# Performance work log

Hardware: AMD Instinct MI355X
Metric: run time of the kernel (lower is better)

## Reference

```python
import jax, jax.numpy as jnp
import numpy as np

N = 128       # SSM state size
L = 32768     # l_max / sequence length
DT_MIN, DT_MAX = 0.001, 0.1


def setup_inputs() -> dict:
    key = jax.random.key(0)
    ku, ka, kb, kc, ks = jax.random.split(key, 5)
    u = jax.random.normal(ku, (L,), dtype=jnp.float32)
    # lecun_normal: std = 1/sqrt(fan_in); shift A by -2I for stability over L powers
    A = jax.random.normal(ka, (N, N), dtype=jnp.float32) * (1.0 / np.sqrt(N)) - 2.0 * jnp.eye(N, dtype=jnp.float32)
    B = jax.random.normal(kb, (N, 1), dtype=jnp.float32)            # fan_in=1 -> std 1
    C = jax.random.normal(kc, (1, N), dtype=jnp.float32) * (1.0 / np.sqrt(N))
    D = jnp.ones((1,), dtype=jnp.float32)
    log_step = jax.random.uniform(ks, (1,), dtype=jnp.float32) * (np.log(DT_MAX) - np.log(DT_MIN)) + np.log(DT_MIN)
    return {"u": u, "A": A, "B": B, "C": C, "D": D, "log_step": log_step}


def discretize(a, b, step):
    # bilinear (Tustin) discretization, identical to the flax module
    i = jnp.eye(a.shape[0], dtype=a.dtype)
    bl = jnp.linalg.inv(i - (step / 2.0) * a)
    ab = bl @ (i + (step / 2.0) * a)
    bb = (bl * step) @ b
    return ab, bb


def k_conv(ab, bb, cb, l):
    # K[t] = cb @ ab^t @ bb  -- same math as the matrix_power list-comp,
    # computed with a single scan carrying x_t = ab^t @ bb  (N,1)
    def step(x, _):
        k_t = (cb @ x).reshape(())
        return ab @ x, k_t
    _, k = jax.lax.scan(step, bb, None, length=l)
    return k  # (l,)


def causal_convolution(u, k):
    l = u.shape[0]
    ud = jnp.fft.rfft(jnp.pad(u, (0, k.shape[0])))
    kd = jnp.fft.rfft(jnp.pad(k, (0, l)))
    return jnp.fft.irfft(ud * kd)[:l]


def reference(u, A, B, C, D, log_step):
    step = jnp.exp(log_step)
    ab, bb = discretize(A, B, step)
    K = k_conv(ab, bb, C, u.shape[0])
    return causal_convolution(u, K) + D * u
```

## Files before the change

kernel.cpp:

```cpp
#include <hip/hip_runtime.h>
#include <math.h>

#define L_SEQ 32768
#define PL 16384
#define GP 16384

typedef unsigned short u16;
typedef float f32x4 __attribute__((ext_vector_type(4)));
typedef short bf16x8 __attribute__((ext_vector_type(8)));
typedef u16 u16x4 __attribute__((ext_vector_type(4)));

__device__ __forceinline__ u16 f2bf(float x) {
  unsigned u = __float_as_uint(x);
  u = u + 0x7FFFu + ((u >> 16) & 1u);
  return (u16)(u >> 16);
}
__device__ __forceinline__ float bf2f(u16 h) {
  return __uint_as_float(((unsigned)h) << 16);
}
__device__ __forceinline__ int MIDX(int r, int c) {
  return (r << 7) + (c ^ ((r & 7) << 3));
}
__device__ __forceinline__ f32x4 MF(bf16x8 a, bf16x8 b, f32x4 c) {
  return __builtin_amdgcn_mfma_f32_16x16x32_bf16(a, b, c, 0, 0, 0);
}

template<int ASRC,int BSRC,int OUTM,int OUTG,int MODE>
__device__ void mm(u16* lds, const u16* gA, int aPl, const u16* gB, int bPl,
                   u16* gO, int oPl, int gOrow0, u16* gO2,
                   int Mrows, int N, float c3, const u16* gE, const u16* gEt) {
  u16* Mh = lds;          u16* Ml = lds + PL;
  u16* Th = lds + 2 * PL; u16* Tl = lds + 3 * PL;
  const int t = threadIdx.x, lane = t & 63;
  const int la = lane & 15, g = lane >> 4;
  const int w = t >> 6;
  const int r0 = (w >> 2) << 5, c0 = (w & 3) << 5;
  constexpr bool doA = (OUTM == 2) || (OUTG == 2) || (OUTG == 3);
  constexpr bool doT = (OUTM == 2) || (OUTG == 1) || (OUTG == 3);
  const bool act = (r0 < Mrows) && (c0 < N);

  __syncthreads();

  f32x4 acc[2][2], accT[2][2];
#pragma unroll
  for (int i = 0; i < 2; ++i)
#pragma unroll
    for (int j = 0; j < 2; ++j) {
      acc[i][j] = (f32x4){0.f, 0.f, 0.f, 0.f};
      accT[i][j] = (f32x4){0.f, 0.f, 0.f, 0.f};
    }

  if (act) {
    bf16x8 Ah[2][2], Al[2][2], Bh[2][2], Bl[2][2];
    auto load_stage = [&](int kb, int s) {
      const int kp = (kb << 5) + (g << 3);
#pragma unroll
      for (int fr = 0; fr < 2; ++fr) {
        const int ar = r0 + (fr << 4) + la;
        if constexpr (ASRC == 0) {
          Ah[s][fr] = *(const bf16x8*)(Mh + MIDX(ar, kp));
          Al[s][fr] = *(const bf16x8*)(Ml + MIDX(ar, kp));
        } else {
          Ah[s][fr] = *(const bf16x8*)(gA + ar * 128 + kp);
          Al[s][fr] = *(const bf16x8*)(gA + aPl + ar * 128 + kp);
        }
      }
#pragma unroll
      for (int fc = 0; fc < 2; ++fc) {
        const int bc = c0 + (fc << 4) + la;
        if constexpr (BSRC == 0) {
          Bh[s][fc] = *(const bf16x8*)(Th + MIDX(bc, kp));
          Bl[s][fc] = *(const bf16x8*)(Tl + MIDX(bc, kp));
        } else {
          Bh[s][fc] = *(const bf16x8*)(gB + bc * 128 + kp);
          Bl[s][fc] = *(const bf16x8*)(gB + bPl + bc * 128 + kp);
        }
      }
    };
    load_stage(0, 0);
#pragma unroll
    for (int kb = 0; kb < 4; ++kb) {
      const int cur = kb & 1;
      if (kb < 3) load_stage(kb + 1, cur ^ 1);
#pragma unroll
      for (int fr = 0; fr < 2; ++fr)
#pragma unroll
        for (int fc = 0; fc < 2; ++fc) {
          if constexpr (doA) {
            acc[fr][fc] = MF(Ah[cur][fr], Bh[cur][fc], acc[fr][fc]);
            acc[fr][fc] = MF(Ah[cur][fr], Bl[cur][fc], acc[fr][fc]);
            acc[fr][fc] = MF(Al[cur][fr], Bh[cur][fc], acc[fr][fc]);
          }
          if constexpr (doT) {
            accT[fr][fc] = MF(Bh[cur][fc], Ah[cur][fr], accT[fr][fc]);
            accT[fr][fc] = MF(Bh[cur][fc], Al[cur][fr], accT[fr][fc]);
            accT[fr][fc] = MF(Bl[cur][fc], Ah[cur][fr], accT[fr][fc]);
          }
        }
    }
  }

  if constexpr (OUTM == 2) __syncthreads();

  if (!act) return;

  if constexpr (doT) {
#pragma unroll
    for (int fr = 0; fr < 2; ++fr)
#pragma unroll
      for (int fc = 0; fc < 2; ++fc) {
        const int rr = r0 + (fr << 4) + la;
        const int cb = c0 + (fc << 4) + (g << 2);
        float v[4];
#pragma unroll
        for (int j = 0; j < 4; ++j) v[j] = accT[fr][fc][j];
        if constexpr (MODE == 2) {
#pragma unroll
          for (int j = 0; j < 4; ++j)
            v[j] += bf2f(gE[rr * 128 + cb + j]) + bf2f(gE[GP + rr * 128 + cb + j])
                  + bf2f(Mh[MIDX(rr, cb + j)]) + bf2f(Ml[MIDX(rr, cb + j)])
                  + ((rr == cb + j) ? 1.f : 0.f);
        }
        if constexpr (MODE == 4) {
#pragma unroll
          for (int j = 0; j < 4; ++j)
            v[j] = c3 * (v[j] + bf2f(gE[rr * 128 + cb + j]) +
                         bf2f(gE[GP + rr * 128 + cb + j])) -
                   ((rr == cb + j) ? 1.f : 0.f);
        }
        u16x4 hi, lo;
#pragma unroll
        for (int j = 0; j < 4; ++j) {
          u16 h = f2bf(v[j]); hi[j] = h; lo[j] = f2bf(v[j] - bf2f(h));
        }
        if constexpr (OUTM == 2) {
          *(u16x4*)(Mh + MIDX(rr, cb)) = hi;
          *(u16x4*)(Ml + MIDX(rr, cb)) = lo;
        }
        if constexpr (OUTG == 1) {
          if (rr < Mrows) {
            *(u16x4*)(gO + (gOrow0 + rr) * 128 + cb) = hi;
            *(u16x4*)(gO + oPl + (gOrow0 + rr) * 128 + cb) = lo;
          }
        }
        if constexpr (OUTG == 3) {
          *(u16x4*)(gO + rr * 128 + cb) = hi;
          *(u16x4*)(gO + oPl + rr * 128 + cb) = lo;
        }
      }
  }
  if constexpr (doA) {
#pragma unroll
    for (int fr = 0; fr < 2; ++fr)
#pragma unroll
      for (int fc = 0; fc < 2; ++fc) {
        const int cc = c0 + (fc << 4) + la;
        const int rb = r0 + (fr << 4) + (g << 2);
        float v[4];
#pragma unroll
        for (int j = 0; j < 4; ++j) v[j] = acc[fr][fc][j];
        if constexpr (MODE == 2) {
#pragma unroll
          for (int j = 0; j < 4; ++j)
            v[j] += bf2f(gE[(rb + j) * 128 + cc]) + bf2f(gE[GP + (rb + j) * 128 + cc])
                  + bf2f(Th[MIDX(cc, rb + j)]) + bf2f(Tl[MIDX(cc, rb + j)])
                  + ((rb + j == cc) ? 1.f : 0.f);
        }
        if constexpr (MODE == 4) {
#pragma unroll
          for (int j = 0; j < 4; ++j)
            v[j] = c3 * (v[j] + bf2f(gEt[cc * 128 + rb + j]) +
                         bf2f(gEt[GP + cc * 128 + rb + j])) -
                   ((rb + j == cc) ? 1.f : 0.f);
        }
        u16x4 hi, lo;
#pragma unroll
        for (int j = 0; j < 4; ++j) {
          u16 h = f2bf(v[j]); hi[j] = h; lo[j] = f2bf(v[j] - bf2f(h));
        }
        if constexpr (OUTM == 2) {
          *(u16x4*)(Th + MIDX(cc, rb)) = hi;
          *(u16x4*)(Tl + MIDX(cc, rb)) = lo;
        }
        if constexpr (OUTG == 2) {
          if (cc < N) {
            *(u16x4*)(gO + (gOrow0 + cc) * 128 + rb) = hi;
            *(u16x4*)(gO + oPl + (gOrow0 + cc) * 128 + rb) = lo;
          }
        }
        if constexpr (OUTG == 3) {
          *(u16x4*)(gO2 + cc * 128 + rb) = hi;
          *(u16x4*)(gO2 + oPl + cc * 128 + rb) = lo;
        }
      }
  }
}

__global__ void __launch_bounds__(1024, 4) chain_k(const float* __restrict__ A,
                                                   const float* __restrict__ Bv,
                                                   const float* __restrict__ Cv,
                                                   const float* __restrict__ lstep,
                                                   u16* ws) {
  extern __shared__ u16 lds[];
  const int bid = blockIdx.x;
  u16* gT    = ws + bid * 131072;
  u16* gU12  = gT + 32768;
  u16* gU12t = gT + 65536;
  u16* rt = ws + 262144;
  u16* gs = ws + 327680;

  const int t = threadIdx.x;
  const float step = expf(lstep[0]);
  const float alpha = 0.5f * step / (1.f + step);
  const float c3 = 2.f / (1.f + step);
  u16* Mh = lds; u16* Ml = lds + PL; u16* Th = lds + 2 * PL; u16* Tl = lds + 3 * PL;

#pragma unroll
  for (int i = 0; i < 4; ++i) {
    int e4 = (t + (i << 10)) << 2;
    int r = e4 >> 7, c = e4 & 127;
    float4 av = *(const float4*)(A + e4);
    float vv[4] = {av.x, av.y, av.z, av.w};
    u16x4 hi, lo;
#pragma unroll
    for (int j = 0; j < 4; ++j) {
      float v = alpha * (vv[j] + ((r == c + j) ? 2.f : 0.f));
      u16 h = f2bf(v); hi[j] = h; lo[j] = f2bf(v - bf2f(h));
    }
    *(u16x4*)(Mh + MIDX(r, c)) = hi;
    *(u16x4*)(Ml + MIDX(r, c)) = lo;
    *(u16x4*)(gT + r * 128 + c) = hi;
    *(u16x4*)(gT + GP + r * 128 + c) = lo;
#pragma unroll
    for (int j = 0; j < 4; ++j) {
      Th[MIDX(c + j, r)] = hi[j];
      Tl[MIDX(c + j, r)] = lo[j];
    }
  }

  mm<0,0,2,0,0>(lds, 0,0, 0,0, 0,0,0,0, 128,128, 0.f, 0,0);
  mm<1,0,0,3,2>(lds, gT,GP, 0,0, gU12,GP,0,gU12t, 128,128, 0.f, gT,0);
  mm<0,0,2,0,0>(lds, 0,0, 0,0, 0,0,0,0, 128,128, 0.f, 0,0);
  mm<1,0,2,0,4>(lds, gU12,GP, 0,0, 0,0,0,0, 128,128, c3, gU12,gU12t);

  if (bid == 0) {
    __syncthreads();
    if (t < 128) {
      float a2 = 0.f;
      for (int p = 0; p < 128; ++p)
        a2 = fmaf(bf2f(Mh[MIDX(t, p)]) + bf2f(Ml[MIDX(t, p)]), Bv[p], a2);
      float v = 0.5f * step * (a2 + Bv[t]);
      u16 h = f2bf(v);
      rt[t] = h;
      rt[32768 + t] = f2bf(v - bf2f(h));
    }
    for (int k = 0; k < 8; ++k) {
      mm<0,1,0,2,0>(lds, 0,0, rt,32768, rt,32768,(1<<k),0, 128,(1<<k), 0.f, 0,0);
      if (k < 7) mm<0,0,2,0,0>(lds, 0,0, 0,0, 0,0,0,0, 128,128, 0.f, 0,0);
    }
  } else {
    __syncthreads();
    if (t < 128) {
      float v = Cv[t];
      u16 h = f2bf(v);
      gs[t] = h;
      gs[GP + t] = f2bf(v - bf2f(h));
    }
    for (int k = 0; k < 8; ++k)
      mm<0,0,2,0,0>(lds, 0,0, 0,0, 0,0,0,0, 128,128, 0.f, 0,0);
    for (int k = 0; k < 7; ++k) {
      mm<1,0,0,1,0>(lds, gs,GP, 0,0, gs,GP,(1<<k),0, (1<<k),128, 0.f, 0,0);
      if (k < 6) mm<0,0,2,0,0>(lds, 0,0, 0,0, 0,0,0,0, 128,128, 0.f, 0,0);
    }
  }
}

__global__ __launch_bounds__(256) void kmat_k(const u16* __restrict__ gs,
                                              const u16* __restrict__ rt,
                                              float* __restrict__ Kv) {
  __shared__ float srow[128];
  int t1 = blockIdx.x, t0 = threadIdx.x;
  if (t0 < 128)
    srow[t0] = bf2f(gs[t1 * 128 + t0]) + bf2f(gs[GP + t1 * 128 + t0]);
  __syncthreads();
  const u16* rh = rt + t0 * 128;
  const u16* rl = rt + 32768 + t0 * 128;
  float acc = 0.f;
#pragma unroll 4
  for (int p = 0; p < 128; p += 8) {
    uint4 qh = *(const uint4*)(rh + p);
    uint4 ql = *(const uint4*)(rl + p);
    unsigned dh[4] = {qh.x, qh.y, qh.z, qh.w};
    unsigned dl[4] = {ql.x, ql.y, ql.z, ql.w};
#pragma unroll
    for (int j = 0; j < 4; ++j) {
      acc = fmaf(srow[p + 2 * j],     bf2f((u16)dh[j]) + bf2f((u16)dl[j]), acc);
      acc = fmaf(srow[p + 2 * j + 1],
                 bf2f((u16)(dh[j] >> 16)) + bf2f((u16)(dl[j] >> 16)), acc);
    }
  }
  Kv[t1 * 256 + t0] = acc;
}

__global__ __launch_bounds__(128) void conv_k(const float* __restrict__ u,
                                              const float* __restrict__ Kv,
                                              float* __restrict__ Pp) {
  __shared__ __align__(16) float ks[512];
  __shared__ __align__(16) float usw[1024];

  int bid = blockIdx.x, tid = threadIdx.x;
  int m = (int)((sqrtf(8.f * (float)bid + 1.f) - 1.f) * 0.5f);
  while ((m + 1) * (m + 2) / 2 <= bid) ++m;
  while (m * (m + 1) / 2 > bid) --m;
  int c = bid - m * (m + 1) / 2;
  int w0 = (m - c - 1) << 9;

  for (int idx = tid; idx < 512; idx += 128) ks[idx] = Kv[(c << 9) + idx];
  for (int idx = tid; idx < 1024; idx += 128) {
    int gi = w0 + idx;
    float v = (gi >= 0) ? u[gi] : 0.f;
    int b = idx >> 2;
    int pb = b ^ ((b >> 3) & 7);
    usw[(pb << 2) | (idx & 3)] = v;
  }
  __syncthreads();

  int tb = tid << 2;

#define LD4(x)                                                      \
  (*(const float4*)&usw[((((x) >> 2) ^ ((((x) >> 2) >> 3) & 7)) << 2)])

  float4 wlo = LD4(508 + tb);
  float4 whi = LD4(512 + tb);
  float acc0 = 0.f, acc1 = 0.f, acc2 = 0.f, acc3 = 0.f;

#pragma unroll 4
  for (int s8 = 0; s8 < 512; s8 += 4) {
    float4 k4 = *(const float4*)&ks[s8];
    acc0 = fmaf(k4.x, whi.x, acc0);
    acc0 = fmaf(k4.y, wlo.w, acc0);
    acc0 = fmaf(k4.z, wlo.z, acc0);
    acc0 = fmaf(k4.w, wlo.y, acc0);
    acc1 = fmaf(k4.x, whi.y, acc1);
    acc1 = fmaf(k4.y, whi.x, acc1);
    acc1 = fmaf(k4.z, wlo.w, acc1);
    acc1 = fmaf(k4.w, wlo.z, acc1);
    acc2 = fmaf(k4.x, whi.z, acc2);
    acc2 = fmaf(k4.y, whi.y, acc2);
    acc2 = fmaf(k4.z, whi.x, acc2);
    acc2 = fmaf(k4.w, wlo.w, acc2);
    acc3 = fmaf(k4.x, whi.w, acc3);
    acc3 = fmaf(k4.y, whi.z, acc3);
    acc3 = fmaf(k4.z, whi.y, acc3);
    acc3 = fmaf(k4.w, whi.x, acc3);
    if (s8 < 508) {
      whi = wlo;
      wlo = LD4(504 + tb - s8);
    }
  }
#undef LD4

  float* dst = Pp + (bid << 9) + tb;
  *(float4*)dst = make_float4(acc0, acc1, acc2, acc3);
}

__global__ __launch_bounds__(256) void reduce_k(const float* __restrict__ Pp,
                                                const float* __restrict__ u,
                                                const float* __restrict__ D,
                                                float* __restrict__ y) {
  int t = blockIdx.x * 256 + threadIdx.x;
  if (t >= L_SEQ) return;
  int m = t >> 9;
  int base = ((m * (m + 1) / 2) << 9) + (t & 511);
  float acc = D[0] * u[t];
  for (int c = 0; c <= m; ++c) acc += Pp[base + (c << 9)];
  y[t] = acc;
}

extern "C" void kernel_launch(void* const* d_in, const int* in_sizes, int n_in,
                              void* d_out, int out_size, void* d_ws, size_t ws_size,
                              hipStream_t stream) {
  (void)in_sizes; (void)n_in; (void)out_size; (void)ws_size;
  const float* u     = (const float*)d_in[0];
  const float* A     = (const float*)d_in[1];
  const float* B     = (const float*)d_in[2];
  const float* C     = (const float*)d_in[3];
  const float* D     = (const float*)d_in[4];
  const float* lstep = (const float*)d_in[5];
  float* y = (float*)d_out;
  u16* ws = (u16*)d_ws;

  u16* rt = ws + 262144;
  u16* gs = ws + 327680;
  float* Kv = (float*)((char*)d_ws + 720896);
  float* Pp = (float*)((char*)d_ws + 851968);

  (void)hipFuncSetAttribute((const void*)chain_k,
                            hipFuncAttributeMaxDynamicSharedMemorySize, 131072);
  hipLaunchKernelGGL(chain_k, dim3(2), dim3(1024), 131072, stream, A, B, C, lstep, ws);
  hipLaunchKernelGGL(kmat_k, dim3(128), dim3(256), 0, stream, gs, rt, Kv);
  hipLaunchKernelGGL(conv_k, dim3(2080), dim3(128), 0, stream, u, Kv, Pp);
  hipLaunchKernelGGL(reduce_k, dim3(L_SEQ / 256), dim3(256), 0, stream, Pp, u, D, y);
}
```

Measured before the change: 214.2 us.

## Restructure SSM kernel chain into single-block fused power ladder and wider conv tiles

The two-block matrix-power chain and the separate kmat kernel are replaced by a single-block chain that interleaves squaring steps with extension products (B-side and C-side powers built by doubling), then computes K directly with MFMA into Kv. This removes one kernel launch and the duplicated squaring work across two blocks. The convolution kernel now computes 16 outputs per thread over 1024-wide output tiles with 64-thread blocks, halving the block count and the partial-sum rows the reduce kernel reads. The cost is that the serial chain now runs on one workgroup and does more dependent steps there, and conv blocks carry higher register pressure.

After: 326.0 us. 52.2% more time.

```diff
diff --git a/kernel.cpp b/kernel.cpp
--- a/kernel.cpp
+++ b/kernel.cpp
@@ -3,7 +3,7 @@
 
 #define L_SEQ 32768
 #define PL 16384
-#define GP 16384
+#define PLG 32768
 
 typedef unsigned short u16;
 typedef float f32x4 __attribute__((ext_vector_type(4)));
@@ -15,184 +15,237 @@
   u = u + 0x7FFFu + ((u >> 16) & 1u);
   return (u16)(u >> 16);
 }
-__device__ __forceinline__ float bf2f(u16 h) {
-  return __uint_as_float(((unsigned)h) << 16);
-}
-__device__ __forceinline__ int MIDX(int r, int c) {
-  return (r << 7) + (c ^ ((r & 7) << 3));
-}
+__device__ __forceinline__ float bf2f(u16 h) { return __uint_as_float(((unsigned)h) << 16); }
+__device__ __forceinline__ int MIDX(int r, int c) { return (r << 7) + (c ^ ((r & 7) << 3)); }
 __device__ __forceinline__ f32x4 MF(bf16x8 a, bf16x8 b, f32x4 c) {
   return __builtin_amdgcn_mfma_f32_16x16x32_bf16(a, b, c, 0, 0, 0);
 }
-
-template<int ASRC,int BSRC,int OUTM,int OUTG,int MODE>
-__device__ void mm(u16* lds, const u16* gA, int aPl, const u16* gB, int bPl,
-                   u16* gO, int oPl, int gOrow0, u16* gO2,
-                   int Mrows, int N, float c3, const u16* gE, const u16* gEt) {
-  u16* Mh = lds;          u16* Ml = lds + PL;
-  u16* Th = lds + 2 * PL; u16* Tl = lds + 3 * PL;
-  const int t = threadIdx.x, lane = t & 63;
-  const int la = lane & 15, g = lane >> 4;
-  const int w = t >> 6;
-  const int r0 = (w >> 2) << 5, c0 = (w & 3) << 5;
-  constexpr bool doA = (OUTM == 2) || (OUTG == 2) || (OUTG == 3);
-  constexpr bool doT = (OUTM == 2) || (OUTG == 1) || (OUTG == 3);
-  const bool act = (r0 < Mrows) && (c0 < N);
+__device__ __forceinline__ void gfrag(const u16* g, int row, int kp, bf16x8& h, bf16x8& l) {
+  h = *(const bf16x8*)(g + row * 128 + kp);
+  l = *(const bf16x8*)(g + PLG + row * 128 + kp);
+}
+__device__ __forceinline__ void lfrag(const u16* base, int row, int kp, bf16x8& h, bf16x8& l) {
+  h = *(const bf16x8*)(base + MIDX(row, kp));
+  l = *(const bf16x8*)(base + PL + MIDX(row, kp));
+}
+__device__ __forceinline__ void pack4(const float* v, u16x4& hi, u16x4& lo) {
+#pragma unroll
+  for (int j = 0; j < 4; ++j) {
+    u16 h = f2bf(v[j]);
+    hi[j] = h;
+    lo[j] = f2bf(v[j] - bf2f(h));
+  }
+}
+
+template<int MK, int ERS, bool HEC, bool M2, bool DUMP>
+__device__ void step(u16* lds,
+                     const u16* gAm, const u16* gBm, const u16* gU, float c3,
+                     float* KvO, int kc0, u16* gDump,
+                     int ER, const u16* gAe, u16* gOe, int eR0,
+                     const u16* gT1, const u16* gT2x,
+                     int EC, const u16* gBe, u16* gOc, int eC0) {
+  u16* Mb = lds;
+  u16* Tb = lds + 2 * PL;
+  const int t = threadIdx.x, lane = t & 63, la = lane & 15, g = lane >> 4;
+  const int w = t >> 6, wr = w >> 2, wc = w & 3;
+  const int r0 = wr << 5, c0 = wc << 5;
+  constexpr int ERN = (ERS > 0) ? ERS : 1;
 
   __syncthreads();
 
-  f32x4 acc[2][2], accT[2][2];
+  f32x4 acc[2][2], accT[2][2], accE[ERN][2], accC[2][2];
 #pragma unroll
   for (int i = 0; i < 2; ++i)
 #pragma unroll
     for (int j = 0; j < 2; ++j) {
       acc[i][j] = (f32x4){0.f, 0.f, 0.f, 0.f};
       accT[i][j] = (f32x4){0.f, 0.f, 0.f, 0.f};
-    }
-
-  if (act) {
-    bf16x8 Ah[2][2], Al[2][2], Bh[2][2], Bl[2][2];
-    auto load_stage = [&](int kb, int s) {
-      const int kp = (kb << 5) + (g << 3);
+      accC[i][j] = (f32x4){0.f, 0.f, 0.f, 0.f};
+    }
+#pragma unroll
+  for (int f = 0; f < ERN; ++f)
+#pragma unroll
+    for (int j = 0; j < 2; ++j) accE[f][j] = (f32x4){0.f, 0.f, 0.f, 0.f};
+
+#pragma unroll
+  for (int kb = 0; kb < 4; ++kb) {
+    const int kp = (kb << 5) + (g << 3);
+    bf16x8 Ah[2], Al[2], Bh[2], Bl[2];
+    if constexpr (MK != 0) {
 #pragma unroll
       for (int fr = 0; fr < 2; ++fr) {
-        const int ar = r0 + (fr << 4) + la;
-        if constexpr (ASRC == 0) {
-          Ah[s][fr] = *(const bf16x8*)(Mh + MIDX(ar, kp));
-          Al[s][fr] = *(const bf16x8*)(Ml + MIDX(ar, kp));
-        } else {
-          Ah[s][fr] = *(const bf16x8*)(gA + ar * 128 + kp);
-          Al[s][fr] = *(const bf16x8*)(gA + aPl + ar * 128 + kp);
-        }
-      }
+        int ar = r0 + (fr << 4) + la;
+        if constexpr (MK == 1) lfrag(Mb, ar, kp, Ah[fr], Al[fr]);
+        else gfrag(gAm, ar, kp, Ah[fr], Al[fr]);
+      }
+    }
+#pragma unroll
+    for (int fc = 0; fc < 2; ++fc) {
+      int bc = c0 + (fc << 4) + la;
+      if constexpr (MK == 3) gfrag(gBm, bc, kp, Bh[fc], Bl[fc]);
+      else lfrag(Tb, bc, kp, Bh[fc], Bl[fc]);
+    }
+    bf16x8 Eh[ERN], El[ERN];
+    if constexpr (ERS > 0) {
+#pragma unroll
+      for (int f = 0; f < ERS; ++f) {
+        int er = (wr << 4) + (f << 6) + la;
+        gfrag(gAe, er, kp, Eh[f], El[f]);
+      }
+    }
+    bf16x8 Fh[2], Fl[2];
+    if constexpr (HEC) {
+#pragma unroll
+      for (int e = 0; e < 2; ++e) {
+        int ec = (wc << 5) + (e << 4) + la;
+        gfrag(gBe, ec, kp, Fh[e], Fl[e]);
+      }
+    }
+    if constexpr (MK == 1 || MK == 2) {
+#pragma unroll
+      for (int fr = 0; fr < 2; ++fr)
+#pragma unroll
+        for (int fc = 0; fc < 2; ++fc) {
+          acc[fr][fc] = MF(Ah[fr], Bh[fc], acc[fr][fc]);
+          acc[fr][fc] = MF(Ah[fr], Bl[fc], acc[fr][fc]);
+          acc[fr][fc] = MF(Al[fr], Bh[fc], acc[fr][fc]);
+          accT[fr][fc] = MF(Bh[fc], Ah[fr], accT[fr][fc]);
+          accT[fr][fc] = MF(Bh[fc], Al[fr], accT[fr][fc]);
+          accT[fr][fc] = MF(Bl[fc], Ah[fr], accT[fr][fc]);
+        }
+    }
+    if constexpr (MK == 3) {
+#pragma unroll
+      for (int fr = 0; fr < 2; ++fr)
+#pragma unroll
+        for (int fc = 0; fc < 2; ++fc) {
+          accT[fr][fc] = MF(Bh[fc], Ah[fr], accT[fr][fc]);
+          accT[fr][fc] = MF(Bh[fc], Al[fr], accT[fr][fc]);
+          accT[fr][fc] = MF(Bl[fc], Ah[fr], accT[fr][fc]);
+        }
+    }
+    if constexpr (ERS > 0) {
+#pragma unroll
+      for (int f = 0; f < ERS; ++f)
+#pragma unroll
+        for (int fc = 0; fc < 2; ++fc) {
+          accE[f][fc] = MF(Bh[fc], Eh[f], accE[f][fc]);
+          accE[f][fc] = MF(Bh[fc], El[f], accE[f][fc]);
+          accE[f][fc] = MF(Bl[fc], Eh[f], accE[f][fc]);
+        }
+    }
+    if constexpr (HEC) {
+#pragma unroll
+      for (int fr = 0; fr < 2; ++fr)
+#pragma unroll
+        for (int e = 0; e < 2; ++e) {
+          accC[fr][e] = MF(Ah[fr], Fh[e], accC[fr][e]);
+          accC[fr][e] = MF(Ah[fr], Fl[e], accC[fr][e]);
+          accC[fr][e] = MF(Al[fr], Fh[e], accC[fr][e]);
+        }
+    }
+  }
+
+  __syncthreads();
+
+  if constexpr (MK == 1 || MK == 2) {
+#pragma unroll
+    for (int fr = 0; fr < 2; ++fr)
 #pragma unroll
       for (int fc = 0; fc < 2; ++fc) {
-        const int bc = c0 + (fc << 4) + la;
-        if constexpr (BSRC == 0) {
-          Bh[s][fc] = *(const bf16x8*)(Th + MIDX(bc, kp));
-          Bl[s][fc] = *(const bf16x8*)(Tl + MIDX(bc, kp));
-        } else {
-          Bh[s][fc] = *(const bf16x8*)(gB + bc * 128 + kp);
-          Bl[s][fc] = *(const bf16x8*)(gB + bPl + bc * 128 + kp);
-        }
-      }
-    };
-    load_stage(0, 0);
-#pragma unroll
-    for (int kb = 0; kb < 4; ++kb) {
-      const int cur = kb & 1;
-      if (kb < 3) load_stage(kb + 1, cur ^ 1);
-#pragma unroll
-      for (int fr = 0; fr < 2; ++fr)
+        int rr = r0 + (fr << 4) + la;
+        int cb = c0 + (fc << 4) + (g << 2);
+        float v[4];
+#pragma unroll
+        for (int j = 0; j < 4; ++j) v[j] = accT[fr][fc][j];
+        if constexpr (MK == 2) {
+#pragma unroll
+          for (int j = 0; j < 4; ++j)
+            v[j] = c3 * (v[j] + bf2f(gU[rr * 128 + cb + j]) +
+                         bf2f(gU[PLG + rr * 128 + cb + j])) -
+                   ((rr == cb + j) ? 1.f : 0.f);
+        }
+        u16x4 hi, lo;
+        pack4(v, hi, lo);
+        *(u16x4*)(Mb + MIDX(rr, cb)) = hi;
+        *(u16x4*)(Mb + PL + MIDX(rr, cb)) = lo;
+        if constexpr (DUMP) {
+          *(u16x4*)(gDump + rr * 128 + cb) = hi;
+          *(u16x4*)(gDump + PLG + rr * 128 + cb) = lo;
+        }
+        int cc = c0 + (fc << 4) + la;
+        int rb = r0 + (fr << 4) + (g << 2);
+        float q[4];
+#pragma unroll
+        for (int j = 0; j < 4; ++j) q[j] = acc[fr][fc][j];
+        if constexpr (MK == 2) {
+#pragma unroll
+          for (int j = 0; j < 4; ++j)
+            q[j] = c3 * (q[j] + bf2f(gU[(rb + j) * 128 + cc]) +
+                         bf2f(gU[PLG + (rb + j) * 128 + cc])) -
+                   ((rb + j == cc) ? 1.f : 0.f);
+        }
+        u16x4 hi2, lo2;
+        pack4(q, hi2, lo2);
+        *(u16x4*)(Tb + MIDX(cc, rb)) = hi2;
+        *(u16x4*)(Tb + PL + MIDX(cc, rb)) = lo2;
+      }
+  }
+  if constexpr (MK == 3) {
+#pragma unroll
+    for (int fr = 0; fr < 2; ++fr)
+#pragma unroll
+      for (int fc = 0; fc < 2; ++fc) {
+        int rr = r0 + (fr << 4) + la;
+        int cb = c0 + (fc << 4) + (g << 2);
+        f32x4 v = accT[fr][fc];
+        *(float4*)(KvO + rr * 256 + kc0 + cb) = make_float4(v[0], v[1], v[2], v[3]);
+      }
+  }
+  if constexpr (ERS > 0) {
+#pragma unroll
+    for (int f = 0; f < ERS; ++f) {
+      int er = (wr << 4) + (f << 6) + la;
+      if (er < ER) {
 #pragma unroll
         for (int fc = 0; fc < 2; ++fc) {
-          if constexpr (doA) {
-            acc[fr][fc] = MF(Ah[cur][fr], Bh[cur][fc], acc[fr][fc]);
-            acc[fr][fc] = MF(Ah[cur][fr], Bl[cur][fc], acc[fr][fc]);
-            acc[fr][fc] = MF(Al[cur][fr], Bh[cur][fc], acc[fr][fc]);
+          int cb = c0 + (fc << 4) + (g << 2);
+          float v[4];
+#pragma unroll
+          for (int j = 0; j < 4; ++j) v[j] = accE[f][fc][j];
+          if constexpr (M2) {
+#pragma unroll
+            for (int j = 0; j < 4; ++j)
+              v[j] += bf2f(gT1[er * 128 + cb + j]) + bf2f(gT1[PLG + er * 128 + cb + j]) +
+                      bf2f(gT2x[er * 128 + cb + j]) + bf2f(gT2x[PLG + er * 128 + cb + j]) +
+                      ((er == cb + j) ? 1.f : 0.f);
           }
-          if constexpr (doT) {
-            accT[fr][fc] = MF(Bh[cur][fc], Ah[cur][fr], accT[fr][fc]);
-            accT[fr][fc] = MF(Bh[cur][fc], Al[cur][fr], accT[fr][fc]);
-            accT[fr][fc] = MF(Bl[cur][fc], Ah[cur][fr], accT[fr][fc]);
-          }
-        }
-    }
-  }
-
-  if constexpr (OUTM == 2) __syncthreads();
-
-  if (!act) return;
-
-  if constexpr (doT) {
-#pragma unroll
-    for (int fr = 0; fr < 2; ++fr)
-#pragma unroll
-      for (int fc = 0; fc < 2; ++fc) {
-        const int rr = r0 + (fr << 4) + la;
-        const int cb = c0 + (fc << 4) + (g << 2);
-        float v[4];
-#pragma unroll
-        for (int j = 0; j < 4; ++j) v[j] = accT[fr][fc][j];
-        if constexpr (MODE == 2) {
-#pragma unroll
-          for (int j = 0; j < 4; ++j)
-            v[j] += bf2f(gE[rr * 128 + cb + j]) + bf2f(gE[GP + rr * 128 + cb + j])
-                  + bf2f(Mh[MIDX(rr, cb + j)]) + bf2f(Ml[MIDX(rr, cb + j)])
-                  + ((rr == cb + j) ? 1.f : 0.f);
-        }
-        if constexpr (MODE == 4) {
-#pragma unroll
-          for (int j = 0; j < 4; ++j)
-            v[j] = c3 * (v[j] + bf2f(gE[rr * 128 + cb + j]) +
-                         bf2f(gE[GP + rr * 128 + cb + j])) -
-                   ((rr == cb + j) ? 1.f : 0.f);
-        }
-        u16x4 hi, lo;
-#pragma unroll
-        for (int j = 0; j < 4; ++j) {
-          u16 h = f2bf(v[j]); hi[j] = h; lo[j] = f2bf(v[j] - bf2f(h));
-        }
-        if constexpr (OUTM == 2) {
-          *(u16x4*)(Mh + MIDX(rr, cb)) = hi;
-          *(u16x4*)(Ml + MIDX(rr, cb)) = lo;
-        }
-        if constexpr (OUTG == 1) {
-          if (rr < Mrows) {
-            *(u16x4*)(gO + (gOrow0 + rr) * 128 + cb) = hi;
-            *(u16x4*)(gO + oPl + (gOrow0 + rr) * 128 + cb) = lo;
-          }
-        }
-        if constexpr (OUTG == 3) {
-          *(u16x4*)(gO + rr * 128 + cb) = hi;
-          *(u16x4*)(gO + oPl + rr * 128 + cb) = lo;
-        }
-      }
-  }
-  if constexpr (doA) {
-#pragma unroll
-    for (int fr = 0; fr < 2; ++fr)
-#pragma unroll
-      for (int fc = 0; fc < 2; ++fc) {
-        const int cc = c0 + (fc << 4) + la;
-        const int rb = r0 + (fr << 4) + (g << 2);
-        float v[4];
-#pragma unroll
-        for (int j = 0; j < 4; ++j) v[j] = acc[fr][fc][j];
-        if constexpr (MODE == 2) {
-#pragma unroll
-          for (int j = 0; j < 4; ++j)
-            v[j] += bf2f(gE[(rb + j) * 128 + cc]) + bf2f(gE[GP + (rb + j) * 128 + cc])
-                  + bf2f(Th[MIDX(cc, rb + j)]) + bf2f(Tl[MIDX(cc, rb + j)])
-                  + ((rb + j == cc) ? 1.f : 0.f);
-        }
-        if constexpr (MODE == 4) {
-#pragma unroll
-          for (int j = 0; j < 4; ++j)
-            v[j] = c3 * (v[j] + bf2f(gEt[cc * 128 + rb + j]) +
-                         bf2f(gEt[GP + cc * 128 + rb + j])) -
-                   ((rb + j == cc) ? 1.f : 0.f);
-        }
-        u16x4 hi, lo;
-#pragma unroll
-        for (int j = 0; j < 4; ++j) {
-          u16 h = f2bf(v[j]); hi[j] = h; lo[j] = f2bf(v[j] - bf2f(h));
-        }
-        if constexpr (OUTM == 2) {
-          *(u16x4*)(Th + MIDX(cc, rb)) = hi;
-          *(u16x4*)(Tl + MIDX(cc, rb)) = lo;
-        }
-        if constexpr (OUTG == 2) {
-          if (cc < N) {
-            *(u16x4*)(gO + (gOrow0 + cc) * 128 + rb) = hi;
-            *(u16x4*)(gO + oPl + (gOrow0 + cc) * 128 + rb) = lo;
-          }
-        }
-        if constexpr (OUTG == 3) {
-          *(u16x4*)(gO2 + cc * 128 + rb) = hi;
-          *(u16x4*)(gO2 + oPl + cc * 128 + rb) = lo;
-        }
-      }
+          u16x4 hi, lo;
+          pack4(v, hi, lo);
+          *(u16x4*)(gOe + (eR0 + er) * 128 + cb) = hi;
+          *(u16x4*)(gOe + PLG + (eR0 + er) * 128 + cb) = lo;
+        }
+      }
+    }
+  }
+  if constexpr (HEC) {
+#pragma unroll
+    for (int e = 0; e < 2; ++e) {
+      int ec = (wc << 5) + (e << 4) + la;
+      if (ec < EC) {
+#pragma unroll
+        for (int fr = 0; fr < 2; ++fr) {
+          int rb = r0 + (fr << 4) + (g << 2);
+          float v[4];
+#pragma unroll
+          for (int j = 0; j < 4; ++j) v[j] = accC[fr][e][j];
+          u16x4 hi, lo;
+          pack4(v, hi, lo);
+          *(u16x4*)(gOc + (eC0 + ec) * 128 + rb) = hi;
+          *(u16x4*)(gOc + PLG + (eC0 + ec) * 128 + rb) = lo;
+        }
+      }
+    }
   }
 }
 
@@ -202,17 +255,17 @@
                                                    const float* __restrict__ lstep,
                                                    u16* ws) {
   extern __shared__ u16 lds[];
-  const int bid = blockIdx.x;
-  u16* gT    = ws + bid * 131072;
-  u16* gU12  = gT + 32768;
-  u16* gU12t = gT + 65536;
-  u16* rt = ws + 262144;
-  u16* gs = ws + 327680;
+  u16* gT  = ws;
+  u16* gT2 = ws + 65536;
+  u16* gU  = ws + 131072;
+  u16* rt  = ws + 196608;
+  u16* gs  = ws + 262144;
+  float* Kv = (float*)(ws + 327680);
 
   const int t = threadIdx.x;
-  const float step = expf(lstep[0]);
-  const float alpha = 0.5f * step / (1.f + step);
-  const float c3 = 2.f / (1.f + step);
+  const float stp = expf(lstep[0]);
+  const float alpha = 0.5f * stp / (1.f + stp);
+  const float c3 = 2.f / (1.f + stp);
   u16* Mh = lds; u16* Ml = lds + PL; u16* Th = lds + 2 * PL; u16* Tl = lds + 3 * PL;
 
 #pragma unroll
@@ -221,16 +274,15 @@
     int r = e4 >> 7, c = e4 & 127;
     float4 av = *(const float4*)(A + e4);
     float vv[4] = {av.x, av.y, av.z, av.w};
+    float tv[4];
+#pragma unroll
+    for (int j = 0; j < 4; ++j) tv[j] = alpha * (vv[j] + ((r == c + j) ? 2.f : 0.f));
     u16x4 hi, lo;
-#pragma unroll
-    for (int j = 0; j < 4; ++j) {
-      float v = alpha * (vv[j] + ((r == c + j) ? 2.f : 0.f));
-      u16 h = f2bf(v); hi[j] = h; lo[j] = f2bf(v - bf2f(h));
-    }
+    pack4(tv, hi, lo);
     *(u16x4*)(Mh + MIDX(r, c)) = hi;
     *(u16x4*)(Ml + MIDX(r, c)) = lo;
     *(u16x4*)(gT + r * 128 + c) = hi;
-    *(u16x4*)(gT + GP + r * 128 + c) = lo;
+    *(u16x4*)(gT + PLG + r * 128 + c) = lo;
 #pragma unroll
     for (int j = 0; j < 4; ++j) {
       Th[MIDX(c + j, r)] = hi[j];
@@ -238,130 +290,106 @@
     }
   }
 
-  mm<0,0,2,0,0>(lds, 0,0, 0,0, 0,0,0,0, 128,128, 0.f, 0,0);
-  mm<1,0,0,3,2>(lds, gT,GP, 0,0, gU12,GP,0,gU12t, 128,128, 0.f, gT,0);
-  mm<0,0,2,0,0>(lds, 0,0, 0,0, 0,0,0,0, 128,128, 0.f, 0,0);
-  mm<1,0,2,0,4>(lds, gU12,GP, 0,0, 0,0,0,0, 128,128, c3, gU12,gU12t);
-
-  if (bid == 0) {
-    __syncthreads();
-    if (t < 128) {
-      float a2 = 0.f;
-      for (int p = 0; p < 128; ++p)
-        a2 = fmaf(bf2f(Mh[MIDX(t, p)]) + bf2f(Ml[MIDX(t, p)]), Bv[p], a2);
-      float v = 0.5f * step * (a2 + Bv[t]);
-      u16 h = f2bf(v);
-      rt[t] = h;
-      rt[32768 + t] = f2bf(v - bf2f(h));
-    }
-    for (int k = 0; k < 8; ++k) {
-      mm<0,1,0,2,0>(lds, 0,0, rt,32768, rt,32768,(1<<k),0, 128,(1<<k), 0.f, 0,0);
-      if (k < 7) mm<0,0,2,0,0>(lds, 0,0, 0,0, 0,0,0,0, 128,128, 0.f, 0,0);
-    }
-  } else {
-    __syncthreads();
-    if (t < 128) {
-      float v = Cv[t];
-      u16 h = f2bf(v);
-      gs[t] = h;
-      gs[GP + t] = f2bf(v - bf2f(h));
-    }
-    for (int k = 0; k < 8; ++k)
-      mm<0,0,2,0,0>(lds, 0,0, 0,0, 0,0,0,0, 128,128, 0.f, 0,0);
-    for (int k = 0; k < 7; ++k) {
-      mm<1,0,0,1,0>(lds, gs,GP, 0,0, gs,GP,(1<<k),0, (1<<k),128, 0.f, 0,0);
-      if (k < 6) mm<0,0,2,0,0>(lds, 0,0, 0,0, 0,0,0,0, 128,128, 0.f, 0,0);
-    }
-  }
-}
-
-__global__ __launch_bounds__(256) void kmat_k(const u16* __restrict__ gs,
-                                              const u16* __restrict__ rt,
-                                              float* __restrict__ Kv) {
-  __shared__ float srow[128];
-  int t1 = blockIdx.x, t0 = threadIdx.x;
-  if (t0 < 128)
-    srow[t0] = bf2f(gs[t1 * 128 + t0]) + bf2f(gs[GP + t1 * 128 + t0]);
+  step<1,0,false,false,true>(lds, 0, 0, 0, 0.f, 0, 0, gT2,
+                             0, 0, 0, 0, 0, 0, 0, 0, 0, 0);
+  step<1,2,false,true,false>(lds, 0, 0, 0, 0.f, 0, 0, 0,
+                             128, gT, gU, 0, gT, gT2, 0, 0, 0, 0);
+  step<2,0,false,false,false>(lds, gU, 0, gU, c3, 0, 0, 0,
+                              0, 0, 0, 0, 0, 0, 0, 0, 0, 0);
+
   __syncthreads();
-  const u16* rh = rt + t0 * 128;
-  const u16* rl = rt + 32768 + t0 * 128;
-  float acc = 0.f;
-#pragma unroll 4
-  for (int p = 0; p < 128; p += 8) {
-    uint4 qh = *(const uint4*)(rh + p);
-    uint4 ql = *(const uint4*)(rl + p);
-    unsigned dh[4] = {qh.x, qh.y, qh.z, qh.w};
-    unsigned dl[4] = {ql.x, ql.y, ql.z, ql.w};
-#pragma unroll
-    for (int j = 0; j < 4; ++j) {
-      acc = fmaf(srow[p + 2 * j],     bf2f((u16)dh[j]) + bf2f((u16)dl[j]), acc);
-      acc = fmaf(srow[p + 2 * j + 1],
-                 bf2f((u16)(dh[j] >> 16)) + bf2f((u16)(dl[j] >> 16)), acc);
-    }
-  }
-  Kv[t1 * 256 + t0] = acc;
-}
-
-__global__ __launch_bounds__(128) void conv_k(const float* __restrict__ u,
-                                              const float* __restrict__ Kv,
-                                              float* __restrict__ Pp) {
+  if (t < 128) {
+    float a2 = 0.f;
+    for (int p = 0; p < 128; ++p)
+      a2 = fmaf(bf2f(Mh[MIDX(t, p)]) + bf2f(Ml[MIDX(t, p)]), Bv[p], a2);
+    float v = 0.5f * stp * (a2 + Bv[t]);
+    u16 h = f2bf(v);
+    rt[t] = h;
+    rt[PLG + t] = f2bf(v - bf2f(h));
+  } else if (t < 256) {
+    float v = Cv[t - 128];
+    u16 h = f2bf(v);
+    gs[t - 128] = h;
+    gs[PLG + t - 128] = f2bf(v - bf2f(h));
+  }
+
+  for (int i = 1; i <= 8; ++i) {
+    int EC = 1 << (i - 1);
+    step<1,0,true,false,false>(lds, 0, 0, 0, 0.f, 0, 0, 0,
+                               0, 0, 0, 0, 0, 0, EC, rt, rt, EC);
+  }
+  for (int i = 9; i <= 14; ++i) {
+    int ER = 1 << (i - 9);
+    step<1,1,false,false,false>(lds, 0, 0, 0, 0.f, 0, 0, 0,
+                                ER, gs, gs, ER, 0, 0, 0, 0, 0, 0);
+  }
+  step<0,1,false,false,false>(lds, 0, 0, 0, 0.f, 0, 0, 0,
+                              64, gs, gs, 64, 0, 0, 0, 0, 0, 0);
+  step<3,0,false,false,false>(lds, gs, rt, 0, 0.f, Kv, 0, 0,
+                              0, 0, 0, 0, 0, 0, 0, 0, 0, 0);
+  step<3,0,false,false,false>(lds, gs, rt + 128 * 128, 0, 0.f, Kv, 128, 0,
+                              0, 0, 0, 0, 0, 0, 0, 0, 0, 0);
+}
+
+__global__ __launch_bounds__(64) void conv_k(const float* __restrict__ u,
+                                             const float* __restrict__ Kv,
+                                             float* __restrict__ Pp) {
   __shared__ __align__(16) float ks[512];
-  __shared__ __align__(16) float usw[1024];
+  __shared__ __align__(16) float usw[1536];
 
   int bid = blockIdx.x, tid = threadIdx.x;
-  int m = (int)((sqrtf(8.f * (float)bid + 1.f) - 1.f) * 0.5f);
-  while ((m + 1) * (m + 2) / 2 <= bid) ++m;
-  while (m * (m + 1) / 2 > bid) --m;
-  int c = bid - m * (m + 1) / 2;
-  int w0 = (m - c - 1) << 9;
-
-  for (int idx = tid; idx < 512; idx += 128) ks[idx] = Kv[(c << 9) + idx];
-  for (int idx = tid; idx < 1024; idx += 128) {
+  int m = (int)((sqrtf(4.f * (float)bid + 1.f) - 1.f) * 0.5f);
+  while ((m + 1) * (m + 2) <= bid) ++m;
+  while (m * (m + 1) > bid) --m;
+  int j = bid - m * (m + 1);
+  int w0 = (m << 10) - (j << 9) - 512;
+
+  for (int idx = tid; idx < 512; idx += 64) ks[idx] = Kv[(j << 9) + idx];
+  for (int idx = tid; idx < 1536; idx += 64) {
     int gi = w0 + idx;
     float v = (gi >= 0) ? u[gi] : 0.f;
-    int b = idx >> 2;
-    int pb = b ^ ((b >> 3) & 7);
+    int b = idx >> 2, pb = b ^ ((b >> 3) & 7);
     usw[(pb << 2) | (idx & 3)] = v;
   }
   __syncthreads();
 
-  int tb = tid << 2;
-
-#define LD4(x)                                                      \
-  (*(const float4*)&usw[((((x) >> 2) ^ ((((x) >> 2) >> 3) & 7)) << 2)])
-
-  float4 wlo = LD4(508 + tb);
-  float4 whi = LD4(512 + tb);
-  float acc0 = 0.f, acc1 = 0.f, acc2 = 0.f, acc3 = 0.f;
-
-#pragma unroll 4
-  for (int s8 = 0; s8 < 512; s8 += 4) {
-    float4 k4 = *(const float4*)&ks[s8];
-    acc0 = fmaf(k4.x, whi.x, acc0);
-    acc0 = fmaf(k4.y, wlo.w, acc0);
-    acc0 = fmaf(k4.z, wlo.z, acc0);
-    acc0 = fmaf(k4.w, wlo.y, acc0);
-    acc1 = fmaf(k4.x, whi.y, acc1);
-    acc1 = fmaf(k4.y, whi.x, acc1);
-    acc1 = fmaf(k4.z, wlo.w, acc1);
-    acc1 = fmaf(k4.w, wlo.z, acc1);
-    acc2 = fmaf(k4.x, whi.z, acc2);
-    acc2 = fmaf(k4.y, whi.y, acc2);
-    acc2 = fmaf(k4.z, whi.x, acc2);
-    acc2 = fmaf(k4.w, wlo.w, acc2);
-    acc3 = fmaf(k4.x, whi.w, acc3);
-    acc3 = fmaf(k4.y, whi.z, acc3);
-    acc3 = fmaf(k4.z, whi.y, acc3);
-    acc3 = fmaf(k4.w, whi.x, acc3);
-    if (s8 < 508) {
-      whi = wlo;
-      wlo = LD4(504 + tb - s8);
+  int tb = tid << 4;
+  float acc[16];
+#pragma unroll
+  for (int z = 0; z < 16; ++z) acc[z] = 0.f;
+
+#define LD4(x) (*(const float4*)&usw[((((x) >> 2) ^ ((((x) >> 2) >> 3) & 7)) << 2)])
+  float wf[20];
+  {
+    float4 a0 = LD4(508 + tb), a1 = LD4(512 + tb), a2 = LD4(516 + tb),
+           a3 = LD4(520 + tb), a4 = LD4(524 + tb);
+    wf[0] = a0.x; wf[1] = a0.y; wf[2] = a0.z; wf[3] = a0.w;
+    wf[4] = a1.x; wf[5] = a1.y; wf[6] = a1.z; wf[7] = a1.w;
+    wf[8] = a2.x; wf[9] = a2.y; wf[10] = a2.z; wf[11] = a2.w;
+    wf[12] = a3.x; wf[13] = a3.y; wf[14] = a3.z; wf[15] = a3.w;
+    wf[16] = a4.x; wf[17] = a4.y; wf[18] = a4.z; wf[19] = a4.w;
+  }
+  for (int q = 0; q < 512; q += 4) {
+    float4 k4 = *(const float4*)&ks[q];
+    float kk[4] = {k4.x, k4.y, k4.z, k4.w};
+#pragma unroll
+    for (int ds = 0; ds < 4; ++ds)
+#pragma unroll
+      for (int oi = 0; oi < 16; ++oi)
+        acc[oi] = fmaf(kk[ds], wf[oi - ds + 4], acc[oi]);
+    if (q < 508) {
+#pragma unroll
+      for (int z = 19; z >= 4; --z) wf[z] = wf[z - 4];
+      float4 nw = LD4(504 + tb - q);
+      wf[0] = nw.x; wf[1] = nw.y; wf[2] = nw.z; wf[3] = nw.w;
     }
   }
 #undef LD4
 
-  float* dst = Pp + (bid << 9) + tb;
-  *(float4*)dst = make_float4(acc0, acc1, acc2, acc3);
+  float* dst = Pp + (bid << 10) + tb;
+#pragma unroll
+  for (int z = 0; z < 16; z += 4)
+    *(float4*)(dst + z) = make_float4(acc[z], acc[z + 1], acc[z + 2], acc[z + 3]);
 }
 
 __global__ __launch_bounds__(256) void reduce_k(const float* __restrict__ Pp,
@@ -370,10 +398,11 @@
                                                 float* __restrict__ y) {
   int t = blockIdx.x * 256 + threadIdx.x;
   if (t >= L_SEQ) return;
-  int m = t >> 9;
-  int base = ((m * (m + 1) / 2) << 9) + (t & 511);
+  int m = t >> 10;
+  int nJ = 2 * (m + 1);
+  const float* base = Pp + ((m * (m + 1)) << 10) + (t & 1023);
   float acc = D[0] * u[t];
-  for (int c = 0; c <= m; ++c) acc += Pp[base + (c << 9)];
+  for (int j = 0; j < nJ; ++j) acc += base[j << 10];
   y[t] = acc;
 }
 
@@ -390,15 +419,12 @@
   float* y = (float*)d_out;
   u16* ws = (u16*)d_ws;
 
-  u16* rt = ws + 262144;
-  u16* gs = ws + 327680;
-  float* Kv = (float*)((char*)d_ws + 720896);
-  float* Pp = (float*)((char*)d_ws + 851968);
+  float* Kv = (float*)((char*)d_ws + 655360);
+  float* Pp = (float*)((char*)d_ws + 786432);
 
   (void)hipFuncSetAttribute((const void*)chain_k,
                             hipFuncAttributeMaxDynamicSharedMemorySize, 131072);
-  hipLaunchKernelGGL(chain_k, dim3(2), dim3(1024), 131072, stream, A, B, C, lstep, ws);
-  hipLaunchKernelGGL(kmat_k, dim3(128), dim3(256), 0, stream, gs, rt, Kv);
-  hipLaunchKernelGGL(conv_k, dim3(2080), dim3(128), 0, stream, u, Kv, Pp);
+  hipLaunchKernelGGL(chain_k, dim3(1), dim3(1024), 131072, stream, A, B, C, lstep, ws);
+  hipLaunchKernelGGL(conv_k, dim3(1056), dim3(64), 0, stream, u, Kv, Pp);
   hipLaunchKernelGGL(reduce_k, dim3(L_SEQ / 256), dim3(256), 0, stream, Pp, u, D, y);
 }
```
